# Kernel tuning notes

Measured on AMD Instinct MI355X. Metric: run time of the kernel, lower is better.

The kernel has to match this reference:

```python
import jax, jax.numpy as jnp
import numpy as np

N_NODES = 100000
N_EDGES = 640000
IN_FEAT = 128
HID_FEAT = 128
OUT_FEAT = 40


def sage_conv(x, src, dst, W_l, W_r, b, n_nodes):
    # PyG SAGEConv (aggr='mean', root_weight=True):
    #   out_i = W_l @ mean_{j in N(i)} x_j + W_r @ x_i + b
    msg = x[src]  # [E, d] gather
    agg = jax.ops.segment_sum(msg, dst, num_segments=n_nodes)  # [N, d]
    cnt = jax.ops.segment_sum(jnp.ones((src.shape[0],), x.dtype), dst,
                              num_segments=n_nodes)
    agg = agg / jnp.maximum(cnt, 1.0)[:, None]  # segment mean
    return agg @ W_l + x @ W_r + b


def setup_inputs() -> dict:
    key = jax.random.key(0)
    ks = jax.random.split(key, 8)
    s = lambda fan_in: 1.0 / np.sqrt(fan_in)
    x = jax.random.normal(ks[0], (N_NODES, IN_FEAT), jnp.float32)
    edge_index = jax.random.randint(ks[1], (2, N_EDGES), 0, N_NODES, jnp.int64)
    W1l = jax.random.normal(ks[2], (IN_FEAT, HID_FEAT), jnp.float32) * s(IN_FEAT)
    W1r = jax.random.normal(ks[3], (IN_FEAT, HID_FEAT), jnp.float32) * s(IN_FEAT)
    b1 = jnp.zeros((HID_FEAT,), jnp.float32)
    W2l = jax.random.normal(ks[4], (HID_FEAT, OUT_FEAT), jnp.float32) * s(HID_FEAT)
    W2r = jax.random.normal(ks[5], (HID_FEAT, OUT_FEAT), jnp.float32) * s(HID_FEAT)
    b2 = jnp.zeros((OUT_FEAT,), jnp.float32)
    return {"x": x, "edge_index": edge_index, "W1l": W1l, "W1r": W1r,
            "b1": b1, "W2l": W2l, "W2r": W2r, "b2": b2}


def reference(x, edge_index, W1l, W1r, b1, W2l, W2r, b2):
    src, dst = edge_index[0], edge_index[1]
    n = x.shape[0]
    h = jax.nn.relu(sage_conv(x, src, dst, W1l, W1r, b1, n))
    # dropout is identity in eval mode
    out = sage_conv(h, src, dst, W2l, W2r, b2, n)
    return jax.nn.log_softmax(out, axis=1)
```

## Files before the change

### kernel.cpp

```cpp
#include <hip/hip_runtime.h>
#include <math.h>

#define NN 100000
#define NE 640000
#define DF 128
#define DOUT 40
#define D2 48

typedef short bf16x8 __attribute__((ext_vector_type(8)));
typedef float f32x4 __attribute__((ext_vector_type(4)));
typedef float f32x2 __attribute__((ext_vector_type(2)));

#if defined(__has_builtin)
#if __has_builtin(__builtin_amdgcn_cvt_pk_f32_fp8) && __has_builtin(__builtin_amdgcn_cvt_pk_fp8_f32)
#define HW_FP8 1
#endif
#endif
#ifndef HW_FP8
#define HW_FP8 0
#endif

__device__ __forceinline__ unsigned short f2bf(float f) {
    unsigned int u = __float_as_uint(f);
    u += 0x7fffu + ((u >> 16) & 1u);
    return (unsigned short)(u >> 16);
}

__device__ __forceinline__ unsigned int f2fp8_manual(float f) {
    unsigned u = __float_as_uint(f);
    unsigned s = (u >> 24) & 0x80u;
    unsigned au = u & 0x7fffffffu;
    if (au > 0x43e00000u) au = 0x43e00000u;
    au += 0x7ffffu + ((au >> 20) & 1u);
    if (au < 0x3c800000u) return s;
    unsigned e = (au >> 23) - 120u;
    return s | (e << 3) | ((au >> 20) & 7u);
}

__device__ __forceinline__ unsigned short f2fp8x2(float x, float y) {
#if HW_FP8
    int v = __builtin_amdgcn_cvt_pk_fp8_f32(x, y, 0, false);
    return (unsigned short)(v & 0xffff);
#else
    return (unsigned short)(f2fp8_manual(x) | (f2fp8_manual(y) << 8));
#endif
}

__device__ __forceinline__ void fp8pair(unsigned short p, float& x, float& y) {
#if HW_FP8
    f32x2 r = __builtin_amdgcn_cvt_pk_f32_fp8((int)(unsigned)p, false);
    x = r.x; y = r.y;
#else
    unsigned lo = p & 0xffu, hi = (p >> 8) & 0xffu;
    x = __uint_as_float(((lo & 0x80u) << 24) | ((lo & 0x7fu) << 20)) * 0x1.0p120f;
    y = __uint_as_float(((hi & 0x80u) << 24) | ((hi & 0x7fu) << 20)) * 0x1.0p120f;
#endif
}

__device__ __forceinline__ void fp8quad(unsigned int q, float& x0, float& y0,
                                        float& x1, float& y1) {
#if HW_FP8
    f32x2 lo = __builtin_amdgcn_cvt_pk_f32_fp8((int)q, false);
    f32x2 hi = __builtin_amdgcn_cvt_pk_f32_fp8((int)q, true);
    x0 = lo.x; y0 = lo.y; x1 = hi.x; y1 = hi.y;
#else
    fp8pair((unsigned short)(q & 0xffffu), x0, y0);
    fp8pair((unsigned short)(q >> 16), x1, y1);
#endif
}

__global__ __launch_bounds__(256) void zero_deg_kernel(int* __restrict__ deg) {
    int i = blockIdx.x * 256 + threadIdx.x;
    if (i < NN) deg[i] = 0;
}

#define MK_HIST 2500
#define MK_CONV (MK_HIST + 6250)
#define MK_W1   (MK_CONV + 16)
#define MK_W2   (MK_W1 + 6)
#define MK_GRID MK_W2

__global__ __launch_bounds__(256) void mega_kernel(const float* __restrict__ x,
                                                   unsigned short* __restrict__ xb,
                                                   unsigned char* __restrict__ xq,
                                                   const float* __restrict__ W1l,
                                                   const float* __restrict__ W1r,
                                                   unsigned short* __restrict__ w1p,
                                                   const float* __restrict__ W2l,
                                                   const float* __restrict__ W2r,
                                                   unsigned short* __restrict__ w2lp,
                                                   unsigned short* __restrict__ w2rp,
                                                   const int* __restrict__ dst,
                                                   int* __restrict__ deg,
                                                   int* __restrict__ rank) {
    const int bid = blockIdx.x;
    const int tid = threadIdx.x;
    if (bid < MK_HIST) {
        int e = bid * 256 + tid;
        if (e < NE) rank[e] = atomicAdd(&deg[dst[e]], 1);
    } else if (bid < MK_CONV) {
        int i = ((bid - MK_HIST) * 256 + tid) * 8;
        float4 a = *reinterpret_cast<const float4*>(x + i);
        float4 b = *reinterpret_cast<const float4*>(x + i + 4);
        uint4 o;
        o.x = (unsigned)f2bf(a.x) | ((unsigned)f2bf(a.y) << 16);
        o.y = (unsigned)f2bf(a.z) | ((unsigned)f2bf(a.w) << 16);
        o.z = (unsigned)f2bf(b.x) | ((unsigned)f2bf(b.y) << 16);
        o.w = (unsigned)f2bf(b.z) | ((unsigned)f2bf(b.w) << 16);
        *reinterpret_cast<uint4*>(xb + (size_t)i) = o;
        unsigned short q0 = f2fp8x2(a.x, a.y);
        unsigned short q1 = f2fp8x2(a.z, a.w);
        unsigned short q2 = f2fp8x2(b.x, b.y);
        unsigned short q3 = f2fp8x2(b.z, b.w);
        uint2 qo;
        qo.x = (unsigned)q0 | ((unsigned)q1 << 16);
        qo.y = (unsigned)q2 | ((unsigned)q3 << 16);
        *reinterpret_cast<uint2*>(xq + (size_t)i) = qo;
    } else if (bid < MK_W1) {
        int t = (bid - MK_CONV) * 256 + tid;
        int lane = t & 63;
        int ct = (t >> 6) & 7;
        int kt = t >> 9;
        int c  = ct * 16 + (lane & 15);
        int k0 = (kt & 3) * 32 + (lane >> 4) * 8;
        const float* W = (kt < 4) ? W1l : W1r;
        unsigned int o[4];
#pragma unroll
        for (int j = 0; j < 4; ++j) {
            unsigned int lo = f2bf(W[(size_t)(k0 + 2 * j) * DF + c]);
            unsigned int hi = f2bf(W[(size_t)(k0 + 2 * j + 1) * DF + c]);
            o[j] = lo | (hi << 16);
        }
        uint4 v; v.x = o[0]; v.y = o[1]; v.z = o[2]; v.w = o[3];
        *reinterpret_cast<uint4*>(w1p + (size_t)t * 8) = v;
    } else {
        int t = (bid - MK_W1) * 256 + tid;
        if (t < 1536) {
            int lane = t & 63;
            int g  = t >> 6;
            int ct = g % 3;
            int kt = g / 3;
            int c  = ct * 16 + (lane & 15);
            int k0 = (kt & 3) * 32 + (lane >> 4) * 8;
            const float* W = (kt < 4) ? W2l : W2r;
            unsigned short* dstp = (kt < 4) ? w2lp : w2rp;
            int slot = ((kt & 3) * 3 + ct) * 64 + lane;
            unsigned int o[4];
#pragma unroll
            for (int j = 0; j < 4; ++j) {
                unsigned int lo = (c < DOUT) ? f2bf(W[(size_t)(k0 + 2 * j) * DOUT + c]) : 0u;
                unsigned int hi = (c < DOUT) ? f2bf(W[(size_t)(k0 + 2 * j + 1) * DOUT + c]) : 0u;
                o[j] = lo | (hi << 16);
            }
            uint4 v; v.x = o[0]; v.y = o[1]; v.z = o[2]; v.w = o[3];
            *reinterpret_cast<uint4*>(dstp + (size_t)slot * 8) = v;
        }
    }
}


__global__ __launch_bounds__(256) void scan_block_kernel(const int* __restrict__ deg,
                                                         int* __restrict__ loc,
                                                         int* __restrict__ part) {
    __shared__ int tmp[256];
    const int t = threadIdx.x;
    const int i = blockIdx.x * 256 + t;
    int v = (i < NN) ? deg[i] : 0;
    tmp[t] = v;
    __syncthreads();
    for (int off = 1; off < 256; off <<= 1) {
        int a = (t >= off) ? tmp[t - off] : 0;
        __syncthreads();
        tmp[t] += a;
        __syncthreads();
    }
    if (i < NN) loc[i] = tmp[t] - v;
    if (t == 255) part[blockIdx.x] = tmp[t];
}

__global__ __launch_bounds__(256) void add_off_kernel(const int* __restrict__ loc,
                                                      const int* __restrict__ part,
                                                      const int* __restrict__ deg,
                                                      int2* __restrict__ ofs2) {
    __shared__ int wsum[4];
    const int bb = blockIdx.x;
    const int t  = threadIdx.x;
    int psum = 0;
    for (int i = t; i < bb; i += 256) psum += part[i];
#pragma unroll
    for (int off = 32; off > 0; off >>= 1) psum += __shfl_down(psum, off);
    if ((t & 63) == 0) wsum[t >> 6] = psum;
    __syncthreads();
    int base = wsum[0] + wsum[1] + wsum[2] + wsum[3];
    int i = bb * 256 + t;
    if (i < NN) {
        int o = loc[i] + base;
        ofs2[i] = make_int2(o, o + deg[i]);
    }
}

__global__ __launch_bounds__(256) void fill_kernel(const int* __restrict__ src,
                                                   const int* __restrict__ dst,
                                                   const int2* __restrict__ ofs2,
                                                   const int* __restrict__ rank,
                                                   int* __restrict__ srcs) {
    int e = blockIdx.x * blockDim.x + threadIdx.x;
    if (e < NE) {
        int d = dst[e];
        srcs[ofs2[d].x + rank[e]] = src[e];
    }
}

__global__ __launch_bounds__(256) void gather_mean_fp8_kernel(const unsigned char* __restrict__ xq,
                                                              const int2* __restrict__ ofs2,
                                                              const int* __restrict__ srcs,
                                                              unsigned short* __restrict__ agg) {
    const int gid    = blockIdx.x * 256 + threadIdx.x;
    const int node   = gid >> 5;
    const int lane32 = threadIdx.x & 31;
    if (node >= NN) return;
    const int2 be = ofs2[node];
    const int b = be.x;
    const int e = be.y;
    const unsigned char* fp = xq + lane32 * 4;

    float a0 = 0.f, a1 = 0.f, a2 = 0.f, a3 = 0.f;
    float c0 = 0.f, c1 = 0.f, c2 = 0.f, c3 = 0.f;

    for (int j = b; j < e; j += 8) {
        int s[8];
#pragma unroll
        for (int k = 0; k < 8; ++k)
            s[k] = (j + k < e) ? srcs[j + k] : -1;
        unsigned int v[8];
#pragma unroll
        for (int k = 0; k < 8; ++k)
            v[k] = ((unsigned)s[k] < (unsigned)NN)
                 ? *reinterpret_cast<const unsigned int*>(fp + (size_t)s[k] * DF) : 0u;
        float x0, y0, x1, y1;
        fp8quad(v[0], x0, y0, x1, y1); a0 += x0; a1 += y0; a2 += x1; a3 += y1;
        fp8quad(v[1], x0, y0, x1, y1); c0 += x0; c1 += y0; c2 += x1; c3 += y1;
        fp8quad(v[2], x0, y0, x1, y1); a0 += x0; a1 += y0; a2 += x1; a3 += y1;
        fp8quad(v[3], x0, y0, x1, y1); c0 += x0; c1 += y0; c2 += x1; c3 += y1;
        fp8quad(v[4], x0, y0, x1, y1); a0 += x0; a1 += y0; a2 += x1; a3 += y1;
        fp8quad(v[5], x0, y0, x1, y1); c0 += x0; c1 += y0; c2 += x1; c3 += y1;
        fp8quad(v[6], x0, y0, x1, y1); a0 += x0; a1 += y0; a2 += x1; a3 += y1;
        fp8quad(v[7], x0, y0, x1, y1); c0 += x0; c1 += y0; c2 += x1; c3 += y1;
    }

    const float sc = 1.0f / fmaxf((float)(e - b), 1.0f);
    float s0 = (a0 + c0) * sc, s1 = (a1 + c1) * sc;
    float s2 = (a2 + c2) * sc, s3 = (a3 + c3) * sc;
    uint2 o;
    o.x = (unsigned)f2bf(s0) | ((unsigned)f2bf(s1) << 16);
    o.y = (unsigned)f2bf(s2) | ((unsigned)f2bf(s3) << 16);
    *reinterpret_cast<uint2*>(agg + (size_t)node * DF + lane32 * 4) = o;
}

#define G_ROWS 64
#define LDSW 136

__global__ __launch_bounds__(256) void gemm1_kernel(const unsigned short* __restrict__ aggb,
                                                    const unsigned short* __restrict__ xb,
                                                    const unsigned short* __restrict__ w1p,
                                                    const unsigned short* __restrict__ w2lp,
                                                    const unsigned short* __restrict__ w2rp,
                                                    const float* __restrict__ b1,
                                                    const float* __restrict__ b2,
                                                    unsigned short* __restrict__ h2b,
                                                    unsigned short* __restrict__ h2rb) {
    __shared__ unsigned short sA[G_ROWS * LDSW];
    __shared__ unsigned short sX[G_ROWS * LDSW];
    const int t = threadIdx.x;
    const int row0 = blockIdx.x * G_ROWS;

    for (int i = t; i < G_ROWS * 16; i += 256) {
        int r = i >> 4, ch = i & 15;
        int sr = row0 + r; if (sr > NN - 1) sr = NN - 1;
        *reinterpret_cast<uint4*>(&sA[r * LDSW + ch * 8]) =
            *reinterpret_cast<const uint4*>(aggb + (size_t)sr * DF + ch * 8);
        *reinterpret_cast<uint4*>(&sX[r * LDSW + ch * 8]) =
            *reinterpret_cast<const uint4*>(xb + (size_t)sr * DF + ch * 8);
    }
    __syncthreads();

    const int lane = t & 63;
    const int w = t >> 6;
    const int lr = lane & 15;
    const int hi = lane >> 4;
    f32x4 acc[8];
#pragma unroll
    for (int i = 0; i < 8; ++i) acc[i] = (f32x4){0.f, 0.f, 0.f, 0.f};

    const int arow = (w * 16 + lr) * LDSW + hi * 8;
#pragma unroll
    for (int half = 0; half < 2; ++half) {
        const unsigned short* base = half ? sX : sA;
#pragma unroll
        for (int kq = 0; kq < 4; ++kq) {
            bf16x8 a = __builtin_bit_cast(bf16x8,
                *reinterpret_cast<const uint4*>(&base[arow + kq * 32]));
            const unsigned short* wp = w1p + (size_t)(((half * 4 + kq) * 8) * 64 + lane) * 8;
#pragma unroll
            for (int ct = 0; ct < 8; ++ct) {
                bf16x8 b = __builtin_bit_cast(bf16x8,
                    *reinterpret_cast<const uint4*>(wp + ct * 512));
                acc[ct] = __builtin_amdgcn_mfma_f32_16x16x32_bf16(a, b, acc[ct], 0, 0, 0);
            }
        }
    }

    unsigned short hreg[8][4];
#pragma unroll
    for (int ct = 0; ct < 8; ++ct) {
        float bias = b1[ct * 16 + lr];
#pragma unroll
        for (int v = 0; v < 4; ++v) {
            hreg[ct][v] = f2bf(fmaxf(acc[ct][v] + bias, 0.f));
        }
    }

    __syncthreads();
#pragma unroll
    for (int ct = 0; ct < 8; ++ct) {
#pragma unroll
        for (int v = 0; v < 4; ++v) {
            sA[(w * 16 + hi * 4 + v) * LDSW + ct * 16 + lr] = hreg[ct][v];
        }
    }
    __syncthreads();

    f32x4 acc2[3], acc3[3];
#pragma unroll
    for (int i = 0; i < 3; ++i) {
        acc2[i] = (f32x4){0.f, 0.f, 0.f, 0.f};
        acc3[i] = (f32x4){0.f, 0.f, 0.f, 0.f};
    }
#pragma unroll
    for (int kq = 0; kq < 4; ++kq) {
        bf16x8 a = __builtin_bit_cast(bf16x8,
            *reinterpret_cast<const uint4*>(&sA[arow + kq * 32]));
        const unsigned short* wpl = w2lp + (size_t)((kq * 3) * 64 + lane) * 8;
        const unsigned short* wpr = w2rp + (size_t)((kq * 3) * 64 + lane) * 8;
#pragma unroll
        for (int ct = 0; ct < 3; ++ct) {
            bf16x8 bl = __builtin_bit_cast(bf16x8,
                *reinterpret_cast<const uint4*>(wpl + ct * 512));
            bf16x8 br = __builtin_bit_cast(bf16x8,
                *reinterpret_cast<const uint4*>(wpr + ct * 512));
            acc2[ct] = __builtin_amdgcn_mfma_f32_16x16x32_bf16(a, bl, acc2[ct], 0, 0, 0);
            acc3[ct] = __builtin_amdgcn_mfma_f32_16x16x32_bf16(a, br, acc3[ct], 0, 0, 0);
        }
    }
#pragma unroll
    for (int ct = 0; ct < 3; ++ct) {
        int col = ct * 16 + lr;
        float bias2 = (col < DOUT) ? b2[col] : 0.f;
#pragma unroll
        for (int v = 0; v < 4; ++v) {
            int row = row0 + w * 16 + hi * 4 + v;
            if (row < NN) {
                h2b[(size_t)row * D2 + col]  = f2bf(acc2[ct][v]);
                h2rb[(size_t)row * D2 + col] = f2bf(acc3[ct][v] + bias2);
            }
        }
    }
}

__global__ __launch_bounds__(256) void gather_finish_kernel(const unsigned short* __restrict__ h2b,
                                                            const unsigned short* __restrict__ h2rb,
                                                            const int2* __restrict__ ofs2,
                                                            const int* __restrict__ srcs,
                                                            float* __restrict__ out) {
    const int gid   = blockIdx.x * 256 + threadIdx.x;
    const int node  = gid >> 5;
    const int lane32 = threadIdx.x & 31;
    if (node >= NN) return;
    const int2 be = ofs2[node];
    const int b = be.x;
    const int e = be.y;
    const bool act = lane32 < 20;
    const unsigned short* fp = h2b + lane32 * 2;

    float ax0 = 0.f, ay0 = 0.f, ax1 = 0.f, ay1 = 0.f;
    float ax2 = 0.f, ay2 = 0.f, ax3 = 0.f, ay3 = 0.f;

    for (int j = b; j < e; j += 8) {
        int s[8];
#pragma unroll
        for (int k = 0; k < 8; ++k)
            s[k] = (j + k < e) ? srcs[j + k] : -1;
        unsigned int v[8];
#pragma unroll
        for (int k = 0; k < 8; ++k)
            v[k] = (act && (unsigned)s[k] < (unsigned)NN)
                 ? *reinterpret_cast<const unsigned int*>(fp + (size_t)s[k] * D2) : 0u;
        ax0 += __uint_as_float(v[0] << 16);  ay0 += __uint_as_float(v[0] & 0xffff0000u);
        ax1 += __uint_as_float(v[1] << 16);  ay1 += __uint_as_float(v[1] & 0xffff0000u);
        ax2 += __uint_as_float(v[2] << 16);  ay2 += __uint_as_float(v[2] & 0xffff0000u);
        ax3 += __uint_as_float(v[3] << 16);  ay3 += __uint_as_float(v[3] & 0xffff0000u);
        ax0 += __uint_as_float(v[4] << 16);  ay0 += __uint_as_float(v[4] & 0xffff0000u);
        ax1 += __uint_as_float(v[5] << 16);  ay1 += __uint_as_float(v[5] & 0xffff0000u);
        ax2 += __uint_as_float(v[6] << 16);  ay2 += __uint_as_float(v[6] & 0xffff0000u);
        ax3 += __uint_as_float(v[7] << 16);  ay3 += __uint_as_float(v[7] & 0xffff0000u);
    }

    const float sc = 1.0f / fmaxf((float)(e - b), 1.0f);
    float a0 = ((ax0 + ax1) + (ax2 + ax3)) * sc;
    float a1 = ((ay0 + ay1) + (ay2 + ay3)) * sc;

    float lv0 = -INFINITY, lv1 = -INFINITY;
    if (act) {
        unsigned int sv = *reinterpret_cast<const unsigned int*>(h2rb + (size_t)node * D2 + lane32 * 2);
        lv0 = a0 + __uint_as_float(sv << 16);
        lv1 = a1 + __uint_as_float(sv & 0xffff0000u);
    }

    float mx = fmaxf(lv0, lv1);
#pragma unroll
    for (int off = 16; off > 0; off >>= 1) mx = fmaxf(mx, __shfl_xor(mx, off));
    float e0 = act ? __expf(lv0 - mx) : 0.f;
    float e1 = act ? __expf(lv1 - mx) : 0.f;
    float s = e0 + e1;
#pragma unroll
    for (int off = 16; off > 0; off >>= 1) s += __shfl_xor(s, off);
    float lz = mx + __logf(s);
    if (act) {
        float2 o = make_float2(lv0 - lz, lv1 - lz);
        *reinterpret_cast<float2*>(out + (size_t)node * DOUT + lane32 * 2) = o;
    }
}

extern "C" void kernel_launch(void* const* d_in, const int* in_sizes, int n_in,
                              void* d_out, int out_size, void* d_ws, size_t ws_size,
                              hipStream_t stream) {
    const float* x   = (const float*)d_in[0];
    const int*   ei  = (const int*)d_in[1];
    const int*   src = ei;
    const int*   dst = ei + NE;
    const float* W1l = (const float*)d_in[2];
    const float* W1r = (const float*)d_in[3];
    const float* b1  = (const float*)d_in[4];
    const float* W2l = (const float*)d_in[5];
    const float* W2r = (const float*)d_in[6];
    const float* b2  = (const float*)d_in[7];
    float* out = (float*)d_out;

    int* ip    = (int*)d_ws;
    int* deg   = ip;
    int* loc   = ip + 100000;
    int* rank  = ip + 200000;
    int* srcs  = ip + 840000;
    int* part  = ip + 1480008;
    int2* ofs2 = (int2*)(ip + 1480520);
    unsigned short* up    = (unsigned short*)(ip + 1680520);
    unsigned short* xb    = up;
    unsigned short* aggb  = up + 12800000;
    unsigned short* h2b   = up + 25600000;
    unsigned short* h2rb  = up + 30400000;
    unsigned short* w1p   = up + 35200000;
    unsigned short* w2lp  = up + 35232768;
    unsigned short* w2rp  = up + 35238912;
    unsigned char*  xq    = (unsigned char*)(up + 35245056);

    zero_deg_kernel<<<391, 256, 0, stream>>>(deg);
    mega_kernel<<<MK_GRID, 256, 0, stream>>>(x, xb, xq, W1l, W1r, w1p,
                                             W2l, W2r, w2lp, w2rp, dst, deg, rank);

    scan_block_kernel<<<391, 256, 0, stream>>>(deg, loc, part);
    add_off_kernel<<<391, 256, 0, stream>>>(loc, part, deg, ofs2);
    fill_kernel<<<(NE + 255) / 256, 256, 0, stream>>>(src, dst, ofs2, rank, srcs);

    gather_mean_fp8_kernel<<<12500, 256, 0, stream>>>(xq, ofs2, srcs, aggb);
    gemm1_kernel<<<1563, 256, 0, stream>>>(aggb, xb, w1p, w2lp, w2rp, b1, b2, h2b, h2rb);
    gather_finish_kernel<<<12500, 256, 0, stream>>>(h2b, h2rb, ofs2, srcs, out);
}
```

Before: 148.1 us.

## Build CSR via two-level partitioned radix sort instead of global atomics

Replaces the global-atomic degree histogram, scan and scatter-fill CSR construction with a two-pass partitioning scheme. Edges are first bucketed into 196 partitions of 512 destination nodes using shared-memory histograms. Each partition is then sorted locally in LDS to produce the offsets and source lists. This is meant to remove contended global atomics and random scattered writes, at the cost of an extra edge buffer, more kernel launches, and only 196 blocks in the local CSR pass.

Result: faster. 135.4 us (-8.6%).

```diff
diff --git a/kernel.cpp b/kernel.cpp
--- a/kernel.cpp
+++ b/kernel.cpp
@@ -6,6 +6,14 @@
 #define DF 128
 #define DOUT 40
 #define D2 48
+
+#define PBITS 9
+#define PSIZE 512
+#define NPART 196
+#define KA_BLOCKS 250
+#define KA_EPB 2560
+#define KA_ITER (KA_EPB / 256)
+#define STAGE_CAP 4096
 
 typedef short bf16x8 __attribute__((ext_vector_type(8)));
 typedef float f32x4 __attribute__((ext_vector_type(4)));
@@ -69,13 +77,11 @@
 #endif
 }
 
-__global__ __launch_bounds__(256) void zero_deg_kernel(int* __restrict__ deg) {
-    int i = blockIdx.x * 256 + threadIdx.x;
-    if (i < NN) deg[i] = 0;
-}
-
-#define MK_HIST 2500
-#define MK_CONV (MK_HIST + 6250)
+__global__ __launch_bounds__(256) void zero_phist_kernel(int* __restrict__ phist) {
+    phist[threadIdx.x] = 0;
+}
+
+#define MK_CONV 6250
 #define MK_W1   (MK_CONV + 16)
 #define MK_W2   (MK_W1 + 6)
 #define MK_GRID MK_W2
@@ -89,17 +95,11 @@
                                                    const float* __restrict__ W2l,
                                                    const float* __restrict__ W2r,
                                                    unsigned short* __restrict__ w2lp,
-                                                   unsigned short* __restrict__ w2rp,
-                                                   const int* __restrict__ dst,
-                                                   int* __restrict__ deg,
-                                                   int* __restrict__ rank) {
+                                                   unsigned short* __restrict__ w2rp) {
     const int bid = blockIdx.x;
     const int tid = threadIdx.x;
-    if (bid < MK_HIST) {
-        int e = bid * 256 + tid;
-        if (e < NE) rank[e] = atomicAdd(&deg[dst[e]], 1);
-    } else if (bid < MK_CONV) {
-        int i = ((bid - MK_HIST) * 256 + tid) * 8;
+    if (bid < MK_CONV) {
+        int i = (bid * 256 + tid) * 8;
         float4 a = *reinterpret_cast<const float4*>(x + i);
         float4 b = *reinterpret_cast<const float4*>(x + i + 4);
         uint4 o;
@@ -158,14 +158,28 @@
     }
 }
 
-
-__global__ __launch_bounds__(256) void scan_block_kernel(const int* __restrict__ deg,
-                                                         int* __restrict__ loc,
-                                                         int* __restrict__ part) {
+__global__ __launch_bounds__(256) void part_hist_kernel(const int* __restrict__ dst,
+                                                        int* __restrict__ phist) {
+    __shared__ int h[256];
+    const int t = threadIdx.x;
+    h[t] = 0;
+    __syncthreads();
+    const int base = blockIdx.x * KA_EPB;
+#pragma unroll
+    for (int k = 0; k < KA_ITER; ++k) {
+        int p = dst[base + k * 256 + t] >> PBITS;
+        atomicAdd(&h[p], 1);
+    }
+    __syncthreads();
+    if (h[t]) atomicAdd(&phist[t], h[t]);
+}
+
+__global__ __launch_bounds__(256) void part_scan_kernel(const int* __restrict__ phist,
+                                                        int* __restrict__ pbase,
+                                                        int* __restrict__ gcur) {
     __shared__ int tmp[256];
     const int t = threadIdx.x;
-    const int i = blockIdx.x * 256 + t;
-    int v = (i < NN) ? deg[i] : 0;
+    int v = (t < NPART) ? phist[t] : 0;
     tmp[t] = v;
     __syncthreads();
     for (int off = 1; off < 256; off <<= 1) {
@@ -174,41 +188,108 @@
         tmp[t] += a;
         __syncthreads();
     }
-    if (i < NN) loc[i] = tmp[t] - v;
-    if (t == 255) part[blockIdx.x] = tmp[t];
-}
-
-__global__ __launch_bounds__(256) void add_off_kernel(const int* __restrict__ loc,
-                                                      const int* __restrict__ part,
-                                                      const int* __restrict__ deg,
-                                                      int2* __restrict__ ofs2) {
-    __shared__ int wsum[4];
-    const int bb = blockIdx.x;
-    const int t  = threadIdx.x;
-    int psum = 0;
-    for (int i = t; i < bb; i += 256) psum += part[i];
-#pragma unroll
-    for (int off = 32; off > 0; off >>= 1) psum += __shfl_down(psum, off);
-    if ((t & 63) == 0) wsum[t >> 6] = psum;
-    __syncthreads();
-    int base = wsum[0] + wsum[1] + wsum[2] + wsum[3];
-    int i = bb * 256 + t;
-    if (i < NN) {
-        int o = loc[i] + base;
-        ofs2[i] = make_int2(o, o + deg[i]);
-    }
-}
-
-__global__ __launch_bounds__(256) void fill_kernel(const int* __restrict__ src,
-                                                   const int* __restrict__ dst,
-                                                   const int2* __restrict__ ofs2,
-                                                   const int* __restrict__ rank,
-                                                   int* __restrict__ srcs) {
-    int e = blockIdx.x * blockDim.x + threadIdx.x;
-    if (e < NE) {
-        int d = dst[e];
-        srcs[ofs2[d].x + rank[e]] = src[e];
-    }
+    int excl = tmp[t] - v;
+    if (t < NPART) { pbase[t] = excl; gcur[t] = excl; }
+    if (t == NPART) pbase[t] = NE;
+}
+
+__global__ __launch_bounds__(256) void part_scatter_kernel(const int* __restrict__ src,
+                                                           const int* __restrict__ dst,
+                                                           int* __restrict__ gcur,
+                                                           uint2* __restrict__ epart) {
+    __shared__ int h[256];
+    __shared__ int lbase[256];
+    __shared__ int gbase[256];
+    __shared__ int cur[256];
+    __shared__ uint2 ed[KA_EPB];
+    const int t = threadIdx.x;
+    h[t] = 0;
+    __syncthreads();
+    const int base = blockIdx.x * KA_EPB;
+    int   ps[KA_ITER];
+    uint2 es[KA_ITER];
+#pragma unroll
+    for (int k = 0; k < KA_ITER; ++k) {
+        int e = base + k * 256 + t;
+        int s = src[e], d = dst[e];
+        es[k] = make_uint2((unsigned)s, (unsigned)d);
+        ps[k] = d >> PBITS;
+        atomicAdd(&h[ps[k]], 1);
+    }
+    __syncthreads();
+    int v = h[t];
+    lbase[t] = v;
+    __syncthreads();
+    for (int off = 1; off < 256; off <<= 1) {
+        int a = (t >= off) ? lbase[t - off] : 0;
+        __syncthreads();
+        lbase[t] += a;
+        __syncthreads();
+    }
+    int excl = lbase[t] - v;
+    lbase[t] = excl;
+    cur[t]   = excl;
+    if (t < NPART && v > 0) gbase[t] = atomicAdd(&gcur[t], v);
+    __syncthreads();
+#pragma unroll
+    for (int k = 0; k < KA_ITER; ++k) {
+        int pos = atomicAdd(&cur[ps[k]], 1);
+        ed[pos] = es[k];
+    }
+    __syncthreads();
+    for (int i = t; i < KA_EPB; i += 256) {
+        uint2 e2 = ed[i];
+        int p = (int)(e2.y >> PBITS);
+        epart[gbase[p] + (i - lbase[p])] = e2;
+    }
+}
+
+__global__ __launch_bounds__(256) void local_csr_kernel(const uint2* __restrict__ epart,
+                                                        const int* __restrict__ pbase,
+                                                        int2* __restrict__ ofs2,
+                                                        int* __restrict__ srcs) {
+    __shared__ int cnt[PSIZE];
+    __shared__ int cur[PSIZE];
+    __shared__ int scantmp[256];
+    __shared__ int stage[STAGE_CAP];
+    const int p = blockIdx.x;
+    const int t = threadIdx.x;
+    const int eb = pbase[p], ee = pbase[p + 1];
+    const int ecount = ee - eb;
+    cnt[t] = 0; cnt[t + 256] = 0;
+    __syncthreads();
+    for (int i = t; i < ecount; i += 256) {
+        int nid = (int)epart[eb + i].y - (p << PBITS);
+        atomicAdd(&cnt[nid], 1);
+    }
+    __syncthreads();
+    int c0 = cnt[2 * t], c1 = cnt[2 * t + 1];
+    int pair = c0 + c1;
+    scantmp[t] = pair;
+    __syncthreads();
+    for (int off = 1; off < 256; off <<= 1) {
+        int a = (t >= off) ? scantmp[t - off] : 0;
+        __syncthreads();
+        scantmp[t] += a;
+        __syncthreads();
+    }
+    int pexcl = scantmp[t] - pair;
+    cur[2 * t]     = pexcl;
+    cur[2 * t + 1] = pexcl + c0;
+    int n0 = (p << PBITS) + 2 * t;
+    if (n0 < NN)     ofs2[n0]     = make_int2(eb + pexcl,      eb + pexcl + c0);
+    if (n0 + 1 < NN) ofs2[n0 + 1] = make_int2(eb + pexcl + c0, eb + pexcl + c0 + c1);
+    __syncthreads();
+    for (int i = t; i < ecount; i += 256) {
+        uint2 e2 = epart[eb + i];
+        int nid = (int)e2.y - (p << PBITS);
+        int slot = atomicAdd(&cur[nid], 1);
+        if (slot < STAGE_CAP) stage[slot] = (int)e2.x;
+        else srcs[eb + slot] = (int)e2.x;
+    }
+    __syncthreads();
+    int lim = (ecount < STAGE_CAP) ? ecount : STAGE_CAP;
+    for (int i = t; i < lim; i += 256) srcs[eb + i] = stage[i];
 }
 
 __global__ __launch_bounds__(256) void gather_mean_fp8_kernel(const unsigned char* __restrict__ xq,
@@ -446,14 +527,14 @@
     const float* b2  = (const float*)d_in[7];
     float* out = (float*)d_out;
 
-    int* ip    = (int*)d_ws;
-    int* deg   = ip;
-    int* loc   = ip + 100000;
-    int* rank  = ip + 200000;
-    int* srcs  = ip + 840000;
-    int* part  = ip + 1480008;
-    int2* ofs2 = (int2*)(ip + 1480520);
-    unsigned short* up    = (unsigned short*)(ip + 1680520);
+    int* ip     = (int*)d_ws;
+    int* phist  = ip;
+    int* pbase  = ip + 256;
+    int* gcur   = ip + 512;
+    int* srcs   = ip + 768;
+    uint2* epart = (uint2*)(ip + 640776);
+    int2*  ofs2  = (int2*)(ip + 1920776);
+    unsigned short* up    = (unsigned short*)(ip + 2120776);
     unsigned short* xb    = up;
     unsigned short* aggb  = up + 12800000;
     unsigned short* h2b   = up + 25600000;
@@ -463,13 +544,14 @@
     unsigned short* w2rp  = up + 35238912;
     unsigned char*  xq    = (unsigned char*)(up + 35245056);
 
-    zero_deg_kernel<<<391, 256, 0, stream>>>(deg);
     mega_kernel<<<MK_GRID, 256, 0, stream>>>(x, xb, xq, W1l, W1r, w1p,
-                                             W2l, W2r, w2lp, w2rp, dst, deg, rank);
-
-    scan_block_kernel<<<391, 256, 0, stream>>>(deg, loc, part);
-    add_off_kernel<<<391, 256, 0, stream>>>(loc, part, deg, ofs2);
-    fill_kernel<<<(NE + 255) / 256, 256, 0, stream>>>(src, dst, ofs2, rank, srcs);
+                                             W2l, W2r, w2lp, w2rp);
+
+    zero_phist_kernel<<<1, 256, 0, stream>>>(phist);
+    part_hist_kernel<<<KA_BLOCKS, 256, 0, stream>>>(dst, phist);
+    part_scan_kernel<<<1, 256, 0, stream>>>(phist, pbase, gcur);
+    part_scatter_kernel<<<KA_BLOCKS, 256, 0, stream>>>(src, dst, gcur, epart);
+    local_csr_kernel<<<NPART, 256, 0, stream>>>(epart, pbase, ofs2, srcs);
 
     gather_mean_fp8_kernel<<<12500, 256, 0, stream>>>(xq, ofs2, srcs, aggb);
     gemm1_kernel<<<1563, 256, 0, stream>>>(aggb, xb, w1p, w2lp, w2rp, b1, b2, h2b, h2rb);
```
